# Kernel optimization log

Measured on AMD Instinct MI355X. Metric: run time of the kernel, lower is better.

The kernel has to match this reference:

```python
import jax, jax.numpy as jnp
import numpy as np

B, L, H, NH, DH, FF, NL, REL = 2, 1024, 256, 8, 32, 1024, 2, 100
SCALE = np.sqrt(DH).astype(np.float32)
EPS = 1e-5


def _ln(x, g, b):
    m = jnp.mean(x, axis=-1, keepdims=True)
    v = jnp.mean(jnp.square(x - m), axis=-1, keepdims=True)
    return (x - m) * jax.lax.rsqrt(v + EPS) * g + b


def setup_inputs() -> dict:
    key = jax.random.key(0)
    ks = jax.random.split(key, 20)
    s = 0.02
    Ek = jax.random.normal(ks[0], (REL, DH), jnp.float32) * s
    Ev = jax.random.normal(ks[1], (REL, DH), jnp.float32) * s
    Ek = Ek.at[0].set(0.0)  # padding_idx=0
    Ev = Ev.at[0].set(0.0)
    return {
        "inputs": jax.random.normal(ks[2], (B, L, H), jnp.float32),
        "Wq": jax.random.normal(ks[3], (NL, H, H), jnp.float32) * s,
        "Wk": jax.random.normal(ks[4], (NL, H, H), jnp.float32) * s,
        "Wv": jax.random.normal(ks[5], (NL, H, H), jnp.float32) * s,
        "Wo": jax.random.normal(ks[6], (NL, H, H), jnp.float32) * s,
        "bo": jnp.zeros((NL, H), jnp.float32),
        "W1": jax.random.normal(ks[7], (NL, H, FF), jnp.float32) * s,
        "b1": jnp.zeros((NL, FF), jnp.float32),
        "W2": jax.random.normal(ks[8], (NL, FF, H), jnp.float32) * s,
        "b2": jnp.zeros((NL, H), jnp.float32),
        "ln1_g": jnp.ones((NL, H), jnp.float32),
        "ln1_b": jnp.zeros((NL, H), jnp.float32),
        "ln2_g": jnp.ones((NL, H), jnp.float32),
        "ln2_b": jnp.zeros((NL, H), jnp.float32),
        "Ek": Ek,
        "Ev": Ev,
        "relations": jax.random.randint(ks[9], (B, L, L), 0, REL, jnp.int32),
        "relations_mask": jax.random.randint(ks[10], (B, L, L), 0, 2, jnp.int32).astype(bool),
    }


def reference(inputs, Wq, Wk, Wv, Wo, bo, W1, b1, W2, b2,
              ln1_g, ln1_b, ln2_g, ln2_b, Ek, Ev, relations, relations_mask):
    # relation embeddings shared across layers and heads: (B,L,L,DH)
    rel_k = Ek[relations]
    rel_v = Ev[relations]
    neg = relations_mask.astype(jnp.float32) * (-1e20)  # (B,L,L)
    x = inputs
    for l in range(NL):
        q = (x @ Wq[l]).reshape(B, L, NH, DH)
        k = (x @ Wk[l]).reshape(B, L, NH, DH)
        v = (x @ Wv[l]).reshape(B, L, NH, DH)
        # scores: q.(k_j + rel_k[i,j]) decomposed to avoid (B,H,L,L,DH)
        e = (jnp.einsum('bihd,bjhd->bhij', q, k)
             + jnp.einsum('bihd,bijd->bhij', q, rel_k)) / SCALE
        e = e + neg[:, None, :, :]
        a = jax.nn.softmax(e, axis=-1)  # (B,NH,L,L)
        o = (jnp.einsum('bhij,bjhd->bihd', a, v)
             + jnp.einsum('bhij,bijd->bihd', a, rel_v)).reshape(B, L, H)
        o = o @ Wo[l] + bo[l]
        x = _ln(x + o, ln1_g[l], ln1_b[l])
        ff = jax.nn.relu(x @ W1[l] + b1[l]) @ W2[l] + b2[l]
        x = _ln(x + ff, ln2_g[l], ln2_b[l])
    return x
```

## Files before the change

kernel.cpp:

```cpp
#include <hip/hip_runtime.h>


typedef unsigned short ushortt;
typedef __attribute__((ext_vector_type(8))) short short8;
typedef __attribute__((ext_vector_type(4))) float f32x4;

__device__ __forceinline__ ushortt f2bf(float f) {
  union { float f; unsigned int u; } c; c.f = f;
  unsigned int r = c.u + 0x7fffu + ((c.u >> 16) & 1u);
  return (ushortt)(r >> 16);
}
__device__ __forceinline__ unsigned int pk2(float a, float b) {
  return (unsigned int)f2bf(a) | ((unsigned int)f2bf(b) << 16);
}

__global__ void wcvt_all_k(const float* __restrict__ Wq, const float* __restrict__ Wk,
                           const float* __restrict__ Wv, const float* __restrict__ Wo,
                           const float* __restrict__ W1, const float* __restrict__ W2,
                           ushortt* __restrict__ wbuf) {
  int i = blockIdx.x * blockDim.x + threadIdx.x;
  int st = gridDim.x * blockDim.x;
  for (; i < 1572864; i += st) {
    int l = (i >= 786432) ? 1 : 0;
    int e = i - (l ? 786432 : 0);
    size_t o_w = (size_t)l * 65536, o_w1 = (size_t)l * 262144;
    float v;
    if (e < 262144) {
      int which = e >> 16;
      int loc = e & 65535;
      int k = loc & 255, n = loc >> 8;
      const float* W = (which == 0) ? Wq : (which == 1) ? Wk : (which == 2) ? Wv : Wo;
      v = W[o_w + ((size_t)k << 8) + n];
    } else if (e < 524288) {
      int loc = e - 262144;
      int k = loc & 255, n = loc >> 8;
      v = W1[o_w1 + ((size_t)k << 10) + n];
    } else {
      int loc = e - 524288;
      int k = loc & 1023, n = loc >> 10;
      v = W2[o_w1 + ((size_t)k << 8) + n];
    }
    wbuf[i] = f2bf(v);
  }
}

__global__ __launch_bounds__(256) void cvt_bf_k(
    const float* __restrict__ in, ushortt* __restrict__ out, int n) {
  int idx = (blockIdx.x * 256 + threadIdx.x) * 8;
  if (idx >= n) return;
  float4 f0 = *(const float4*)(in + idx);
  float4 f1 = *(const float4*)(in + idx + 4);
  uint4 u;
  u.x = pk2(f0.x, f0.y); u.y = pk2(f0.z, f0.w);
  u.z = pk2(f1.x, f1.y); u.w = pk2(f1.z, f1.w);
  *(uint4*)(out + idx) = u;
}

__global__ __launch_bounds__(256) void relpack_k(
    const int* __restrict__ rel, const int* __restrict__ msk,
    unsigned char* __restrict__ relc,
    const float* __restrict__ Ev, float* __restrict__ EvT) {
  int g = blockIdx.x * blockDim.x + threadIdx.x;
  const int4* r4 = (const int4*)rel;
  const int4* m4 = (const int4*)msk;
  int4 r = r4[g];
  int4 m = m4[g];
  unsigned int pk = (unsigned int)((m.x ? 128 : r.x) & 255)
                  | ((unsigned int)((m.y ? 128 : r.y) & 255) << 8)
                  | ((unsigned int)((m.z ? 128 : r.z) & 255) << 16)
                  | ((unsigned int)((m.w ? 128 : r.w) & 255) << 24);
  ((unsigned int*)relc)[g] = pk;
  if (g < 3200) {
    int d = g / 100, rr = g - d * 100;
    EvT[d * 100 + rr] = Ev[(rr << 5) + d];
  }
}

__device__ __forceinline__ void mgemm_body(
    const ushortt* __restrict__ A, const ushortt* __restrict__ BT,
    const float* __restrict__ bias, size_t boff,
    float* __restrict__ C, ushortt* __restrict__ cbf,
    int m0, int n0, int N, int K, int kbeg, int kend, int relu, int kvmode)
{
  __shared__ ushortt As[64 * 72];
  __shared__ ushortt Bs[64 * 72];
  int tid = threadIdx.x;
  int wv = tid >> 6, lane = tid & 63;
  int quad = lane >> 4, mr = lane & 15;
  int sm = tid >> 2, k16 = (tid & 3) << 4;

  const ushortt* ap = A + (size_t)(m0 + sm) * K + k16;
  const ushortt* bp = BT + (size_t)(n0 + sm) * K + k16;

  uint4 ra0 = *(const uint4*)(ap + kbeg);
  uint4 ra1 = *(const uint4*)(ap + kbeg + 8);
  uint4 rb0 = *(const uint4*)(bp + kbeg);
  uint4 rb1 = *(const uint4*)(bp + kbeg + 8);

  f32x4 acc[4] = {};
  for (int k0 = kbeg; k0 < kend; k0 += 64) {
    *(uint4*)(&As[sm * 72 + k16])     = ra0;
    *(uint4*)(&As[sm * 72 + k16 + 8]) = ra1;
    *(uint4*)(&Bs[sm * 72 + k16])     = rb0;
    *(uint4*)(&Bs[sm * 72 + k16 + 8]) = rb1;
    __syncthreads();
    if (k0 + 64 < kend) {
      ra0 = *(const uint4*)(ap + k0 + 64);
      ra1 = *(const uint4*)(ap + k0 + 72);
      rb0 = *(const uint4*)(bp + k0 + 64);
      rb1 = *(const uint4*)(bp + k0 + 72);
    }
#pragma unroll
    for (int kh = 0; kh < 2; ++kh) {
      short8 af = *(const short8*)(&As[(wv * 16 + mr) * 72 + (kh << 5) + quad * 8]);
#pragma unroll
      for (int nt = 0; nt < 4; ++nt) {
        short8 bf = *(const short8*)(&Bs[(nt * 16 + mr) * 72 + (kh << 5) + quad * 8]);
        acc[nt] = __builtin_amdgcn_mfma_f32_16x16x32_bf16(af, bf, acc[nt], 0, 0, 0);
      }
    }
    __syncthreads();
  }
#pragma unroll
  for (int nt = 0; nt < 4; ++nt) {
#pragma unroll
    for (int r = 0; r < 4; ++r) {
      int m = m0 + wv * 16 + quad * 4 + r;
      int n = n0 + nt * 16 + mr;
      float v = acc[nt][r];
      if (bias) v += bias[boff + n];
      if (relu) v = fmaxf(v, 0.f);
      if (kvmode == 1) {
        int b = m >> 10, i = m & 1023, h = n >> 5, d = n & 31;
        cbf[(size_t)(((b << 3) + h) * 32 + d) * 1024 + i] = f2bf(v);
      } else if (kvmode == 2) {
        int b = m >> 10, i = m & 1023, h = n >> 5, d = n & 31;
        cbf[(size_t)(((b << 3) + h) * 1024 + i) * 32 + d] = f2bf(v);
      } else if (cbf) {
        cbf[(size_t)m * N + n] = f2bf(v);
      } else {
        C[(size_t)m * N + n] = v;
      }
    }
  }
}

__global__ __launch_bounds__(256) void mgemm_k(
    const ushortt* __restrict__ A, const ushortt* __restrict__ BT,
    const float* __restrict__ bias, size_t boff,
    float* __restrict__ C0, float* __restrict__ C1, ushortt* __restrict__ cbf,
    int N, int K, int relu)
{
  int kidx = blockIdx.z;
  int kc = K / gridDim.z;
  int kbeg = kidx * kc;
  mgemm_body(A, BT, kidx ? nullptr : bias, boff,
             kidx ? C1 : C0, cbf,
             blockIdx.y * 64, blockIdx.x * 64, N, K, kbeg, kbeg + kc, relu, 0);
}

__global__ __launch_bounds__(256) void mqkv_k(
    const ushortt* __restrict__ xbf, const ushortt* __restrict__ WT,
    float* __restrict__ q, ushortt* __restrict__ kbf, ushortt* __restrict__ vTbf)
{
  int sel = blockIdx.x >> 2;
  const ushortt* BT = WT + (size_t)sel * 65536;
  int mode = (sel == 1) ? 2 : (sel == 2) ? 1 : 0;
  mgemm_body(xbf, BT, nullptr, 0,
             (sel == 0) ? q : nullptr,
             (sel == 1) ? kbf : (sel == 2) ? vTbf : nullptr,
             blockIdx.y * 64, (blockIdx.x & 3) * 64, 256, 256, 0, 256, 0, mode);
}

__global__ __launch_bounds__(256) void attn_mf8_k(
    const float* __restrict__ q, const ushortt* __restrict__ kbf,
    const ushortt* __restrict__ vTbf, const float* __restrict__ Ek,
    const float* __restrict__ EvT, const unsigned char* __restrict__ relc,
    ushortt* __restrict__ out)
{
  __shared__ ushortt pbf[8 * 1028];
  __shared__ float regA[1072];
  __shared__ float wbin[8 * 108];
  __shared__ float denom4[32];
  __shared__ uint4 rcs4[512];

  unsigned char* rcs = (unsigned char*)rcs4;
  int tid = threadIdx.x;
  int wv = tid >> 6, lane = tid & 63;
  int quad = lane >> 4, mr = lane & 15;
  int tile = blockIdx.x & 127;
  int h = (blockIdx.x >> 7) & 7;
  int b = blockIdx.x >> 10;
  int i0 = tile << 3;

  float* qs = regA;
  float* expq = regA + 264;

  const uint4* rg = (const uint4*)(relc + (((size_t)b * 1024 + i0) << 10));
  uint4 rc0 = rg[tid];
  uint4 rc1 = rg[256 + tid];
  {
    int i = tid >> 5, d = tid & 31;
    qs[i * 33 + d] = q[(((size_t)(b * 1024 + i0 + i) * 8 + h) << 5) + d]
                     * 0.17677669529663687f;
  }
  for (int p = tid; p < 864; p += 256) wbin[p] = 0.f;
  rcs4[tid] = rc0;
  rcs4[256 + tid] = rc1;
  __syncthreads();

  for (int p = tid; p < 800; p += 256) {
    int i = p / 100, r = p - i * 100;
    const float* ep = Ek + (r << 5);
    float s = 0.f;
#pragma unroll
    for (int d = 0; d < 32; ++d) s += qs[i * 33 + d] * ep[d];
    expq[i * 101 + r] = __expf(s);
  }
  __syncthreads();

  short8 qf;
#pragma unroll
  for (int jj = 0; jj < 8; ++jj)
    ((ushortt*)&qf)[jj] = f2bf(qs[(mr & 7) * 33 + quad * 8 + jj]);

  const ushortt* ks = kbf + ((size_t)(b * 8 + h) << 15);
  const ushortt* vs = vTbf + ((size_t)(b * 8 + h) << 15);

  float psum[4] = {0.f, 0.f, 0.f, 0.f};
  int jbase = (wv * 16) << 4;
  short8 kfa = *(const short8*)(ks + ((size_t)(jbase + mr) << 5) + quad * 8);
  short8 kfb = *(const short8*)(ks + ((size_t)(jbase + 16 + mr) << 5) + quad * 8);
  int iq = (quad & 1) << 2;
  int jofs = ((quad >> 1) << 4) + mr;
#pragma unroll
  for (int t = 0; t < 8; ++t) {
    int j0 = jbase + (t << 5);
    short8 ka = kfa, kb = kfb;
    if (t < 7) {
      kfa = *(const short8*)(ks + ((size_t)(j0 + 32 + mr) << 5) + quad * 8);
      kfb = *(const short8*)(ks + ((size_t)(j0 + 48 + mr) << 5) + quad * 8);
    }
    f32x4 z = {};
    f32x4 sa = __builtin_amdgcn_mfma_f32_16x16x32_bf16(qf, ka, z, 0, 0, 0);
    f32x4 sb = __builtin_amdgcn_mfma_f32_16x16x32_bf16(qf, kb, z, 0, 0, 0);
    int j = j0 + jofs;
#pragma unroll
    for (int r = 0; r < 4; ++r) {
      int i = iq + r;
      float sv = (quad >= 2) ? sb[r] : sa[r];
      unsigned int c = rcs[i * 1024 + j];
      float p = 0.f;
      if (c < 128u) {
        p = __expf(sv) * expq[i * 101 + (int)c];
        atomicAdd(&wbin[i * 108 + (int)c], p);
      }
      psum[r] += p;
      pbf[i * 1028 + j] = f2bf(p);
    }
  }
#pragma unroll
  for (int r = 0; r < 4; ++r) {
    float s = psum[r];
    s += __shfl_xor(s, 1, 64);
    s += __shfl_xor(s, 2, 64);
    s += __shfl_xor(s, 4, 64);
    s += __shfl_xor(s, 8, 64);
    s += __shfl_xor(s, 32, 64);
    if (mr == 0 && quad < 2) denom4[wv * 8 + quad * 4 + r] = s;
  }
  __syncthreads();

  float* pvpart = regA;
  float* pvtot  = regA + 256;
  int d0 = (wv & 1) << 4;
  int k0 = (wv >> 1) << 9;
  int prow = (mr & 7) * 1028;
  f32x4 acc0 = {}, acc1 = {};
  short8 vf = *(const short8*)(vs + ((size_t)(d0 + mr) << 10) + k0 + quad * 8);
#pragma unroll
  for (int kt = 0; kt < 16; ++kt) {
    int kk = k0 + (kt << 5);
    short8 vcur = vf;
    if (kt < 15)
      vf = *(const short8*)(vs + ((size_t)(d0 + mr) << 10) + k0 + ((kt + 1) << 5) + quad * 8);
    short8 pf = *(const short8*)(&pbf[prow + kk + quad * 8]);
    if (kt & 1)
      acc1 = __builtin_amdgcn_mfma_f32_16x16x32_bf16(pf, vcur, acc1, 0, 0, 0);
    else
      acc0 = __builtin_amdgcn_mfma_f32_16x16x32_bf16(pf, vcur, acc0, 0, 0, 0);
  }
  f32x4 acc;
#pragma unroll
  for (int r = 0; r < 4; ++r) acc[r] = acc0[r] + acc1[r];
  if (wv >= 2 && quad < 2) {
#pragma unroll
    for (int r = 0; r < 4; ++r)
      pvpart[((wv & 1) << 7) + (quad * 4 + r) * 16 + mr] = acc[r];
  }
  __syncthreads();
  if (wv < 2 && quad < 2) {
#pragma unroll
    for (int r = 0; r < 4; ++r) {
      int i = quad * 4 + r;
      pvtot[i * 32 + d0 + mr] = acc[r] + pvpart[((wv & 1) << 7) + i * 16 + mr];
    }
  }
  __syncthreads();

  {
    int i = tid >> 5, d = tid & 31;
    const float4* evt = (const float4*)(EvT + d * 100);
    const float4* wb4 = (const float4*)(&wbin[i * 108]);
    float e0 = 0.f, e1 = 0.f, e2 = 0.f, e3 = 0.f;
#pragma unroll
    for (int rq = 0; rq < 25; ++rq) {
      float4 e4 = evt[rq];
      float4 w4 = wb4[rq];
      e0 += w4.x * e4.x;
      e1 += w4.y * e4.y;
      e2 += w4.z * e4.z;
      e3 += w4.w * e4.w;
    }
    float ev = (e0 + e1) + (e2 + e3);
    float den = denom4[i] + denom4[8 + i] + denom4[16 + i] + denom4[24 + i];
    out[(((size_t)(b * 1024 + i0 + i) * 8 + h) << 5) + d] =
        f2bf((pvtot[i * 32 + d] + ev) / den);
  }
}

__global__ __launch_bounds__(256) void ln_k(
    const float* __restrict__ x, const float* __restrict__ o,
    const float* __restrict__ o2,
    const float* __restrict__ g, const float* __restrict__ bta, size_t eoff,
    float* __restrict__ xo, ushortt* __restrict__ xbf, float* __restrict__ fout)
{
  __shared__ float red[256];
  int row = blockIdx.x, t = threadIdx.x;
  size_t idx = (size_t)row * 256 + t;
  float r = x[idx] + o[idx];
  if (o2) r += o2[idx];
  red[t] = r;
  __syncthreads();
  for (int off = 128; off > 0; off >>= 1) {
    if (t < off) red[t] += red[t + off];
    __syncthreads();
  }
  float mean = red[0] * (1.f / 256.f);
  __syncthreads();
  float dv = r - mean;
  red[t] = dv * dv;
  __syncthreads();
  for (int off = 128; off > 0; off >>= 1) {
    if (t < off) red[t] += red[t + off];
    __syncthreads();
  }
  float var = red[0] * (1.f / 256.f);
  float val = dv * rsqrtf(var + 1e-5f) * g[eoff + t] + bta[eoff + t];
  xo[idx] = val;
  xbf[idx] = f2bf(val);
  if (fout) fout[idx] = val;
}

extern "C" void kernel_launch(void* const* d_in, const int* in_sizes, int n_in,
                              void* d_out, int out_size, void* d_ws, size_t ws_size,
                              hipStream_t stream) {
  const float* inp  = (const float*)d_in[0];
  const float* Wq   = (const float*)d_in[1];
  const float* Wk   = (const float*)d_in[2];
  const float* Wv   = (const float*)d_in[3];
  const float* Wo   = (const float*)d_in[4];
  const float* bo   = (const float*)d_in[5];
  const float* W1   = (const float*)d_in[6];
  const float* b1   = (const float*)d_in[7];
  const float* W2   = (const float*)d_in[8];
  const float* b2   = (const float*)d_in[9];
  const float* ln1g = (const float*)d_in[10];
  const float* ln1b = (const float*)d_in[11];
  const float* ln2g = (const float*)d_in[12];
  const float* ln2b = (const float*)d_in[13];
  const float* Ek   = (const float*)d_in[14];
  const float* Ev   = (const float*)d_in[15];
  const int*   rel  = (const int*)d_in[16];
  const int*   msk  = (const int*)d_in[17];

  const size_t SZ = 524288;
  float* x        = (float*)d_ws;
  float* q        = x + SZ;
  ushortt* kbf    = (ushortt*)(q + SZ);
  ushortt* vTbf   = kbf + SZ;
  ushortt* attnbf = vTbf + SZ;
  ushortt* xbf    = attnbf + SZ;
  float* tmp      = (float*)(xbf + SZ);
  ushortt* wbuf   = (ushortt*)(tmp + SZ);
  unsigned char* relc = (unsigned char*)(wbuf + 1572864);
  float* EvT      = (float*)(relc + 2097152);
  float* tmp2     = (float*)((char*)EvT + 16384);
  ushortt* inpbf  = (ushortt*)tmp2;
  ushortt* ffh    = (ushortt*)q;

  dim3 blk(256);
  wcvt_all_k<<<3072, blk, 0, stream>>>(Wq, Wk, Wv, Wo, W1, W2, wbuf);
  relpack_k<<<2048, blk, 0, stream>>>(rel, msk, relc, Ev, EvT);
  cvt_bf_k<<<256, blk, 0, stream>>>(inp, inpbf, 524288);

  for (int l = 0; l < 2; ++l) {
    size_t o_b  = (size_t)l * 256;
    size_t o_b1 = (size_t)l * 1024;
    const ushortt* xinbf = (l == 0) ? inpbf : xbf;
    const float* xin = (l == 0) ? inp : x;
    ushortt* wl = wbuf + (size_t)l * 786432;

    mqkv_k<<<dim3(12, 32), blk, 0, stream>>>(xinbf, wl, q, kbf, vTbf);

    attn_mf8_k<<<2048, blk, 0, stream>>>(q, kbf, vTbf, Ek, EvT, relc, attnbf);

    mgemm_k<<<dim3(4, 32, 2), blk, 0, stream>>>(attnbf, wl + 196608,
                                                bo, o_b, tmp, tmp2, nullptr,
                                                256, 256, 0);
    ln_k<<<2048, blk, 0, stream>>>(xin, tmp, tmp2, ln1g, ln1b, o_b, x, xbf, nullptr);

    mgemm_k<<<dim3(16, 32, 1), blk, 0, stream>>>(xbf, wl + 262144,
                                                 b1, o_b1, nullptr, nullptr, ffh,
                                                 1024, 256, 1);
    mgemm_k<<<dim3(4, 32, 2), blk, 0, stream>>>(ffh, wl + 524288,
                                                b2, o_b, tmp, tmp2, nullptr,
                                                256, 1024, 0);
    ln_k<<<2048, blk, 0, stream>>>(x, tmp, tmp2, ln2g, ln2b, o_b, x, xbf,
                                   (l == 1) ? (float*)d_out : nullptr);
  }
}
```

Baseline: 377.2 us.

## Pack relation codes in MFMA-fragment order and derive softmax denominator from bins

The relation-code packing kernel now writes codes in a tiled layout, 8 rows interleaved per column, so each attention lane loads its four row codes as one 32-bit word straight into registers. This removes the LDS staging of relation codes and the byte reads from LDS. The softmax denominator is now the sum of the per-relation weight bins, which replaces the psum accumulation, the shuffle reductions and the denom shared array. The cost is byte-scattered, uncoalesced writes in the one-time pack kernel, and the new denominator sums the bins in a different order than before.

After: 387.5 us. 1.03x slower.

```diff
diff --git a/kernel.cpp b/kernel.cpp
--- a/kernel.cpp
+++ b/kernel.cpp
@@ -58,18 +58,22 @@
 
 __global__ __launch_bounds__(256) void relpack_k(
     const int* __restrict__ rel, const int* __restrict__ msk,
-    unsigned char* __restrict__ relc,
+    unsigned char* __restrict__ relc2,
     const float* __restrict__ Ev, float* __restrict__ EvT) {
   int g = blockIdx.x * blockDim.x + threadIdx.x;
   const int4* r4 = (const int4*)rel;
   const int4* m4 = (const int4*)msk;
   int4 r = r4[g];
   int4 m = m4[g];
-  unsigned int pk = (unsigned int)((m.x ? 128 : r.x) & 255)
-                  | ((unsigned int)((m.y ? 128 : r.y) & 255) << 8)
-                  | ((unsigned int)((m.z ? 128 : r.z) & 255) << 16)
-                  | ((unsigned int)((m.w ? 128 : r.w) & 255) << 24);
-  ((unsigned int*)relc)[g] = pk;
+  int b = g >> 18;
+  int rem = g & 262143;
+  int i = rem >> 8;
+  int j4 = (rem & 255) << 2;
+  size_t base = ((size_t)b << 20) + ((size_t)(i >> 3) << 13) + (i & 7);
+  relc2[base + ((size_t)(j4 + 0) << 3)] = (unsigned char)(m.x ? 128 : r.x);
+  relc2[base + ((size_t)(j4 + 1) << 3)] = (unsigned char)(m.y ? 128 : r.y);
+  relc2[base + ((size_t)(j4 + 2) << 3)] = (unsigned char)(m.z ? 128 : r.z);
+  relc2[base + ((size_t)(j4 + 3) << 3)] = (unsigned char)(m.w ? 128 : r.w);
   if (g < 3200) {
     int d = g / 100, rr = g - d * 100;
     EvT[d * 100 + rr] = Ev[(rr << 5) + d];
@@ -175,16 +179,13 @@
 __global__ __launch_bounds__(256) void attn_mf8_k(
     const float* __restrict__ q, const ushortt* __restrict__ kbf,
     const ushortt* __restrict__ vTbf, const float* __restrict__ Ek,
-    const float* __restrict__ EvT, const unsigned char* __restrict__ relc,
+    const float* __restrict__ EvT, const unsigned char* __restrict__ relc2,
     ushortt* __restrict__ out)
 {
   __shared__ ushortt pbf[8 * 1028];
   __shared__ float regA[1072];
   __shared__ float wbin[8 * 108];
-  __shared__ float denom4[32];
-  __shared__ uint4 rcs4[512];
-
-  unsigned char* rcs = (unsigned char*)rcs4;
+
   int tid = threadIdx.x;
   int wv = tid >> 6, lane = tid & 63;
   int quad = lane >> 4, mr = lane & 15;
@@ -193,20 +194,26 @@
   int b = blockIdx.x >> 10;
   int i0 = tile << 3;
 
+  int iqsel = quad & 1;
+  int iq = iqsel << 2;
+  int jofs = ((quad >> 1) << 4) + mr;
+  int jbase = wv << 8;
+  const unsigned int* rc2 =
+      (const unsigned int*)(relc2 + (((size_t)(b << 7) + tile) << 13));
+  unsigned int rcw[8];
+#pragma unroll
+  for (int t = 0; t < 8; ++t)
+    rcw[t] = rc2[(((jbase + (t << 5) + jofs)) << 1) + iqsel];
+
   float* qs = regA;
   float* expq = regA + 264;
 
-  const uint4* rg = (const uint4*)(relc + (((size_t)b * 1024 + i0) << 10));
-  uint4 rc0 = rg[tid];
-  uint4 rc1 = rg[256 + tid];
   {
     int i = tid >> 5, d = tid & 31;
     qs[i * 33 + d] = q[(((size_t)(b * 1024 + i0 + i) * 8 + h) << 5) + d]
                      * 0.17677669529663687f;
   }
   for (int p = tid; p < 864; p += 256) wbin[p] = 0.f;
-  rcs4[tid] = rc0;
-  rcs4[256 + tid] = rc1;
   __syncthreads();
 
   for (int p = tid; p < 800; p += 256) {
@@ -227,12 +234,8 @@
   const ushortt* ks = kbf + ((size_t)(b * 8 + h) << 15);
   const ushortt* vs = vTbf + ((size_t)(b * 8 + h) << 15);
 
-  float psum[4] = {0.f, 0.f, 0.f, 0.f};
-  int jbase = (wv * 16) << 4;
   short8 kfa = *(const short8*)(ks + ((size_t)(jbase + mr) << 5) + quad * 8);
   short8 kfb = *(const short8*)(ks + ((size_t)(jbase + 16 + mr) << 5) + quad * 8);
-  int iq = (quad & 1) << 2;
-  int jofs = ((quad >> 1) << 4) + mr;
 #pragma unroll
   for (int t = 0; t < 8; ++t) {
     int j0 = jbase + (t << 5);
@@ -245,29 +248,19 @@
     f32x4 sa = __builtin_amdgcn_mfma_f32_16x16x32_bf16(qf, ka, z, 0, 0, 0);
     f32x4 sb = __builtin_amdgcn_mfma_f32_16x16x32_bf16(qf, kb, z, 0, 0, 0);
     int j = j0 + jofs;
+    unsigned int w = rcw[t];
 #pragma unroll
     for (int r = 0; r < 4; ++r) {
       int i = iq + r;
       float sv = (quad >= 2) ? sb[r] : sa[r];
-      unsigned int c = rcs[i * 1024 + j];
+      unsigned int c = (w >> (r << 3)) & 255u;
       float p = 0.f;
       if (c < 128u) {
         p = __expf(sv) * expq[i * 101 + (int)c];
         atomicAdd(&wbin[i * 108 + (int)c], p);
       }
-      psum[r] += p;
       pbf[i * 1028 + j] = f2bf(p);
     }
-  }
-#pragma unroll
-  for (int r = 0; r < 4; ++r) {
-    float s = psum[r];
-    s += __shfl_xor(s, 1, 64);
-    s += __shfl_xor(s, 2, 64);
-    s += __shfl_xor(s, 4, 64);
-    s += __shfl_xor(s, 8, 64);
-    s += __shfl_xor(s, 32, 64);
-    if (mr == 0 && quad < 2) denom4[wv * 8 + quad * 4 + r] = s;
   }
   __syncthreads();
 
@@ -313,17 +306,18 @@
     const float4* evt = (const float4*)(EvT + d * 100);
     const float4* wb4 = (const float4*)(&wbin[i * 108]);
     float e0 = 0.f, e1 = 0.f, e2 = 0.f, e3 = 0.f;
+    float s0 = 0.f, s1 = 0.f, s2 = 0.f, s3 = 0.f;
 #pragma unroll
     for (int rq = 0; rq < 25; ++rq) {
       float4 e4 = evt[rq];
       float4 w4 = wb4[rq];
-      e0 += w4.x * e4.x;
-      e1 += w4.y * e4.y;
-      e2 += w4.z * e4.z;
-      e3 += w4.w * e4.w;
+      e0 += w4.x * e4.x; s0 += w4.x;
+      e1 += w4.y * e4.y; s1 += w4.y;
+      e2 += w4.z * e4.z; s2 += w4.z;
+      e3 += w4.w * e4.w; s3 += w4.w;
     }
     float ev = (e0 + e1) + (e2 + e3);
-    float den = denom4[i] + denom4[8 + i] + denom4[16 + i] + denom4[24 + i];
+    float den = (s0 + s1) + (s2 + s3);
     out[(((size_t)(b * 1024 + i0 + i) * 8 + h) << 5) + d] =
         f2bf((pvtot[i * 32 + d] + ev) / den);
   }
@@ -393,15 +387,15 @@
   ushortt* xbf    = attnbf + SZ;
   float* tmp      = (float*)(xbf + SZ);
   ushortt* wbuf   = (ushortt*)(tmp + SZ);
-  unsigned char* relc = (unsigned char*)(wbuf + 1572864);
-  float* EvT      = (float*)(relc + 2097152);
+  unsigned char* relc2 = (unsigned char*)(wbuf + 1572864);
+  float* EvT      = (float*)(relc2 + 2097152);
   float* tmp2     = (float*)((char*)EvT + 16384);
   ushortt* inpbf  = (ushortt*)tmp2;
   ushortt* ffh    = (ushortt*)q;
 
   dim3 blk(256);
   wcvt_all_k<<<3072, blk, 0, stream>>>(Wq, Wk, Wv, Wo, W1, W2, wbuf);
-  relpack_k<<<2048, blk, 0, stream>>>(rel, msk, relc, Ev, EvT);
+  relpack_k<<<2048, blk, 0, stream>>>(rel, msk, relc2, Ev, EvT);
   cvt_bf_k<<<256, blk, 0, stream>>>(inp, inpbf, 524288);
 
   for (int l = 0; l < 2; ++l) {
@@ -413,7 +407,7 @@
 
     mqkv_k<<<dim3(12, 32), blk, 0, stream>>>(xinbf, wl, q, kbf, vTbf);
 
-    attn_mf8_k<<<2048, blk, 0, stream>>>(q, kbf, vTbf, Ek, EvT, relc, attnbf);
+    attn_mf8_k<<<2048, blk, 0, stream>>>(q, kbf, vTbf, Ek, EvT, relc2, attnbf);
 
     mgemm_k<<<dim3(4, 32, 2), blk, 0, stream>>>(attnbf, wl + 196608,
                                                 bo, o_b, tmp, tmp2, nullptr,
```
